# Performance work log

Measured on AMD Instinct MI355X. Metric: run time of the kernel, lower is better.

The kernel has to match this reference:

```python
import jax, jax.numpy as jnp
import numpy as np


def setup_inputs() -> dict:
    key = jax.random.key(0)
    ks = jax.random.split(key, 9)
    B = 1024
    s = 0.05
    return {
        "x": jax.random.normal(ks[0], (B, 1024), dtype=jnp.float32),
        "u1": jax.random.normal(ks[1], (8, 8, 16), dtype=jnp.float32) * s,
        "u2": jax.random.normal(ks[2], (8, 8, 16), dtype=jnp.float32) * s,
        "u3": jax.random.normal(ks[3], (16, 16, 16), dtype=jnp.float32) * s,
        "b2": jax.random.normal(ks[4], (16, 16, 16), dtype=jnp.float32) * s,
        "b1_core": jax.random.normal(ks[5], (16, 16), dtype=jnp.float32) * s,
        "bias1": jax.random.normal(ks[6], (8, 8, 16), dtype=jnp.float32) * s,
        "fc2_w": jax.random.normal(ks[7], (10, 1024), dtype=jnp.float32) * s,
        "fc2_b": jax.random.normal(ks[8], (10,), dtype=jnp.float32) * s,
    }


def reference(x, u1, u2, u3, b2, b1_core, bias1, fc2_w, fc2_b):
    batch = x.shape[0]
    t = x.reshape(batch, 8, 8, 16)                       # z a b c
    t = jnp.einsum('zabc,ade->zbcde', t, u1)             # (z,8,16,8,16)
    t = jnp.einsum('zabcd,def->zabcef', t, b2)           # (z,8,16,8,16,16)
    t = jnp.einsum('zabcde,afd->zbcef', t, u2)           # (z,16,8,16,8)
    t = jnp.einsum('zabcd,ce->zabde', t, b1_core)        # (z,16,8,8,16)
    t = jnp.einsum('zabcd,aed->zbce', t, u3)             # (z,8,8,16)
    t = t + bias1
    h = jax.nn.relu(t.reshape(batch, 1024))
    return h @ fc2_w.T + fc2_b
```

## Files before the change

kernel.cpp:

```cpp
#include <hip/hip_runtime.h>


using s16x8 = __attribute__((ext_vector_type(8))) short;
using f32x4 = __attribute__((ext_vector_type(4))) float;

__device__ inline short f2bf(float f) {
    unsigned u = __builtin_bit_cast(unsigned, f);
    u += 0x7fffu + ((u >> 16) & 1u);
    return (short)(u >> 16);
}

__global__ __launch_bounds__(256) void k_prep(
    const float* __restrict__ u1, const float* __restrict__ u2,
    const float* __restrict__ u3, const float* __restrict__ b2,
    const float* __restrict__ b1c, const float* __restrict__ fc2b,
    short* __restrict__ Wb, float* __restrict__ out) {
    const int blk = blockIdx.x;
    const int tid = threadIdx.x;

    __shared__ float b1s[256];
    __shared__ float u1s[128];
    __shared__ float u2s[64 * 17];
    __shared__ float u3s[4096];
    __shared__ float C2t[256 * 17];
    __shared__ float T1s[2048];
    __shared__ float T2s[64 * 17];
    const int d = blk >> 5;
    const int r = (blk >> 2) & 7;
    const int t0 = (blk & 3) * 4;

    if (tid < 40) {
        int idx = blk * 40 + tid;
        out[idx] = fc2b[idx % 10];
    }

    b1s[tid] = b1c[tid];
    {
        float4* dst = (float4*)u3s;
        const float4* src = (const float4*)u3;
#pragma unroll
        for (int q = 0; q < 4; ++q) dst[tid + 256 * q] = src[tid + 256 * q];
    }
    if (tid < 64) {
        const float4* src = (const float4*)&u2[tid * 16];
#pragma unroll
        for (int q = 0; q < 4; ++q) {
            float4 v = src[q];
            u2s[tid * 17 + q * 4 + 0] = v.x;
            u2s[tid * 17 + q * 4 + 1] = v.y;
            u2s[tid * 17 + q * 4 + 2] = v.z;
            u2s[tid * 17 + q * 4 + 3] = v.w;
        }
    }
    if (tid < 8) {
#pragma unroll
        for (int e = 0; e < 16; ++e)
            u1s[tid * 16 + e] = u1[(tid * 8 + d) * 16 + e];
    }
    float b2r[16];
    {
        const float4* src = (const float4*)&b2[tid * 16];
#pragma unroll
        for (int q = 0; q < 4; ++q) {
            float4 v = src[q];
            b2r[q * 4 + 0] = v.x; b2r[q * 4 + 1] = v.y;
            b2r[q * 4 + 2] = v.z; b2r[q * 4 + 3] = v.w;
        }
    }
    __syncthreads();

    {
        float accs[16] = {};
#pragma unroll
        for (int q = 0; q < 16; ++q) {
            const float bq = b2r[q];
#pragma unroll
            for (int s = 0; s < 16; ++s) accs[s] += bq * b1s[q * 16 + s];
        }
#pragma unroll
        for (int s = 0; s < 16; ++s) C2t[tid * 17 + s] = accs[s];
    }
    __syncthreads();

    {
        const int p = tid >> 4, s = tid & 15;
#pragma unroll
        for (int a = 0; a < 8; ++a) {
            float acc = 0.f;
#pragma unroll
            for (int e = 0; e < 16; ++e)
                acc += u1s[a * 16 + e] * C2t[(e * 16 + p) * 17 + s];
            T1s[a * 256 + tid] = acc;
        }
    }
    __syncthreads();

#pragma unroll
    for (int j = 0; j < 4; ++j) {
        int idx = tid + 256 * j;
        int ab = idx >> 4, s = idx & 15;
        int a = ab >> 3, b = ab & 7;
        float acc = 0.f;
#pragma unroll
        for (int p = 0; p < 16; ++p)
            acc += T1s[a * 256 + p * 16 + s] * u2s[(b * 8 + r) * 17 + p];
        T2s[ab * 17 + s] = acc;
    }
    __syncthreads();

    {
        const int j = tid >> 6;
        const int t = t0 + j;
        const int col0 = (tid & 63) * 16;
        const int ab = col0 >> 4;
        const float* t2p = &T2s[ab * 17];
        short* wrow = &Wb[(blk * 4 + j) * 1024 + col0];
        s16x8 v0, v1;
#pragma unroll
        for (int c = 0; c < 16; ++c) {
            const float* u3p = &u3s[c * 256 + t * 16];
            float acc = 0.f;
#pragma unroll
            for (int s = 0; s < 16; ++s) acc += t2p[s] * u3p[s];
            short bf = f2bf(acc);
            if (c < 8) v0[c] = bf; else v1[c - 8] = bf;
        }
        *(s16x8*)(wrow) = v0;
        *(s16x8*)(wrow + 8) = v1;
    }
}

#define LDK 264

__global__ __launch_bounds__(1024) void k_gemm(
    const float* __restrict__ X, const short* __restrict__ Wb,
    const float* __restrict__ bias, const float* __restrict__ W2,
    float* __restrict__ out) {
    extern __shared__ char dsm[];
    short (*As)[LDK] = (short(*)[LDK])dsm;
    short (*Bs)[LDK] = (short(*)[LDK])(dsm + 64 * LDK * 2);
    float* Hpf = (float*)dsm;
    __shared__ float W2s[10][64];

    const int tid = threadIdx.x;
    const int lane = tid & 63;
    const int w = tid >> 6;
    const int g = w >> 2;
    const int wr = (w >> 1) & 1, wc = w & 1;
    const int o0 = blockIdx.x * 64, z0 = blockIdx.y * 64;
    const int lr = lane & 15, lk = lane >> 4;

    if (tid < 160) {
        const int j = tid >> 4, c = (tid & 15) * 4;
        *(float4*)&W2s[j][c] = *(const float4*)&W2[j * 1024 + o0 + c];
    }

    const int srow = tid >> 4;
    const int scol = (tid & 15) * 16;
    const float* xp = &X[(z0 + srow) * 1024 + scol];
    const short* wp = &Wb[(o0 + srow) * 1024 + scol];

    f32x4 acc[2][2] = {};

    for (int it = 0; it < 4; ++it) {
        {
            const float* xi = xp + it * 256;
            const short* wi = wp + it * 256;
#pragma unroll
            for (int h = 0; h < 2; ++h) {
                float4 f0 = *(const float4*)(xi + h * 8);
                float4 f1 = *(const float4*)(xi + h * 8 + 4);
                s16x8 v;
                v[0] = f2bf(f0.x); v[1] = f2bf(f0.y);
                v[2] = f2bf(f0.z); v[3] = f2bf(f0.w);
                v[4] = f2bf(f1.x); v[5] = f2bf(f1.y);
                v[6] = f2bf(f1.z); v[7] = f2bf(f1.w);
                *(s16x8*)&As[srow][scol + h * 8] = v;
                *(s16x8*)&Bs[srow][scol + h * 8] = *(const s16x8*)(wi + h * 8);
            }
        }
        __syncthreads();
#pragma unroll
        for (int ks = 0; ks < 2; ++ks) {
            const int kb = g * 64 + ks * 32 + lk * 8;
            s16x8 a0 = *(const s16x8*)&As[wr * 32 + lr][kb];
            s16x8 a1 = *(const s16x8*)&As[wr * 32 + 16 + lr][kb];
            s16x8 b0 = *(const s16x8*)&Bs[wc * 32 + lr][kb];
            s16x8 b1 = *(const s16x8*)&Bs[wc * 32 + 16 + lr][kb];
            acc[0][0] = __builtin_amdgcn_mfma_f32_16x16x32_bf16(a0, b0, acc[0][0], 0, 0, 0);
            acc[0][1] = __builtin_amdgcn_mfma_f32_16x16x32_bf16(a0, b1, acc[0][1], 0, 0, 0);
            acc[1][0] = __builtin_amdgcn_mfma_f32_16x16x32_bf16(a1, b0, acc[1][0], 0, 0, 0);
            acc[1][1] = __builtin_amdgcn_mfma_f32_16x16x32_bf16(a1, b1, acc[1][1], 0, 0, 0);
        }
        __syncthreads();
    }

#pragma unroll
    for (int m = 0; m < 2; ++m)
#pragma unroll
        for (int n = 0; n < 2; ++n) {
            const int row = wr * 32 + m * 16 + lk * 4;
            const int col = wc * 32 + n * 16 + lr;
#pragma unroll
            for (int j = 0; j < 4; ++j)
                Hpf[(g * 64 + row + j) * 64 + col] = acc[m][n][j];
        }
    __syncthreads();

    const int hrow = tid >> 4;
    const int c4 = (tid & 15) * 4;
    float4 h0 = *(float4*)&Hpf[(0 * 64 + hrow) * 64 + c4];
    float4 h1 = *(float4*)&Hpf[(1 * 64 + hrow) * 64 + c4];
    float4 h2 = *(float4*)&Hpf[(2 * 64 + hrow) * 64 + c4];
    float4 h3 = *(float4*)&Hpf[(3 * 64 + hrow) * 64 + c4];
    float4 bv = *(const float4*)&bias[o0 + c4];
    float hv[4];
    hv[0] = fmaxf(h0.x + h1.x + h2.x + h3.x + bv.x, 0.f);
    hv[1] = fmaxf(h0.y + h1.y + h2.y + h3.y + bv.y, 0.f);
    hv[2] = fmaxf(h0.z + h1.z + h2.z + h3.z + bv.z, 0.f);
    hv[3] = fmaxf(h0.w + h1.w + h2.w + h3.w + bv.w, 0.f);

    float part[10];
#pragma unroll
    for (int jj = 0; jj < 10; ++jj) {
        part[jj] = hv[0] * W2s[jj][c4 + 0] + hv[1] * W2s[jj][c4 + 1]
                 + hv[2] * W2s[jj][c4 + 2] + hv[3] * W2s[jj][c4 + 3];
    }
#pragma unroll
    for (int jj = 0; jj < 10; ++jj) {
        float p = part[jj];
        p += __shfl_xor(p, 1);
        p += __shfl_xor(p, 2);
        p += __shfl_xor(p, 4);
        p += __shfl_xor(p, 8);
        if ((lane & 15) == 0) atomicAdd(&out[(z0 + hrow) * 10 + jj], p);
    }
}

extern "C" void kernel_launch(void* const* d_in, const int* in_sizes, int n_in,
                              void* d_out, int out_size, void* d_ws, size_t ws_size,
                              hipStream_t stream) {
    const float* x     = (const float*)d_in[0];
    const float* u1    = (const float*)d_in[1];
    const float* u2    = (const float*)d_in[2];
    const float* u3    = (const float*)d_in[3];
    const float* b2    = (const float*)d_in[4];
    const float* b1c   = (const float*)d_in[5];
    const float* bias1 = (const float*)d_in[6];
    const float* fc2w  = (const float*)d_in[7];
    const float* fc2b  = (const float*)d_in[8];
    float* out = (float*)d_out;

    short* Wb = (short*)d_ws;

    k_prep<<<256, 256, 0, stream>>>(u1, u2, u3, b2, b1c, fc2b, Wb, out);
    k_gemm<<<dim3(16, 16), 1024, 64 * LDK * 2 * 2, stream>>>(x, Wb, bias1,
                                                             fc2w, out);
}
```

Before: 32.16 us.

## Pre-convert x to swizzled bf16 and double-buffer GEMM with direct global-to-LDS loads

New measurement: 30.28 us. 5.9% less time.

```diff
diff --git a/kernel.cpp b/kernel.cpp
--- a/kernel.cpp
+++ b/kernel.cpp
@@ -10,13 +10,40 @@
     return (short)(u >> 16);
 }
 
+__device__ inline void gload16(const short* g, short* l) {
+    __builtin_amdgcn_global_load_lds(
+        (__attribute__((address_space(1))) void*)g,
+        (__attribute__((address_space(3))) void*)l, 16, 0, 0);
+}
+
 __global__ __launch_bounds__(256) void k_prep(
-    const float* __restrict__ u1, const float* __restrict__ u2,
-    const float* __restrict__ u3, const float* __restrict__ b2,
-    const float* __restrict__ b1c, const float* __restrict__ fc2b,
-    short* __restrict__ Wb, float* __restrict__ out) {
+    const float* __restrict__ x, const float* __restrict__ u1,
+    const float* __restrict__ u2, const float* __restrict__ u3,
+    const float* __restrict__ b2, const float* __restrict__ b1c,
+    const float* __restrict__ fc2b, short* __restrict__ Wb,
+    short* __restrict__ Xb, float* __restrict__ out) {
     const int blk = blockIdx.x;
     const int tid = threadIdx.x;
+
+    if (blk >= 256) {
+        const int base = (blk - 256) * 4096 + tid * 16;
+        const int z = base >> 10;
+        const int col = base & 1023;
+        const int c = col >> 3, g = c >> 4, c4 = c & 15, mz = z & 15;
+        short* xbase = &Xb[z * 1024 + g * 128];
+#pragma unroll
+        for (int h = 0; h < 2; ++h) {
+            float4 f0 = *(const float4*)&x[base + h * 8];
+            float4 f1 = *(const float4*)&x[base + h * 8 + 4];
+            s16x8 v;
+            v[0] = f2bf(f0.x); v[1] = f2bf(f0.y);
+            v[2] = f2bf(f0.z); v[3] = f2bf(f0.w);
+            v[4] = f2bf(f1.x); v[5] = f2bf(f1.y);
+            v[6] = f2bf(f1.z); v[7] = f2bf(f1.w);
+            *(s16x8*)(xbase + ((c4 + h) ^ mz) * 8) = v;
+        }
+        return;
+    }
 
     __shared__ float b1s[256];
     __shared__ float u1s[128];
@@ -110,11 +137,11 @@
 
     {
         const int j = tid >> 6;
+        const int o = blk * 4 + j;
         const int t = t0 + j;
         const int col0 = (tid & 63) * 16;
         const int ab = col0 >> 4;
         const float* t2p = &T2s[ab * 17];
-        short* wrow = &Wb[(blk * 4 + j) * 1024 + col0];
         s16x8 v0, v1;
 #pragma unroll
         for (int c = 0; c < 16; ++c) {
@@ -125,115 +152,103 @@
             short bf = f2bf(acc);
             if (c < 8) v0[c] = bf; else v1[c - 8] = bf;
         }
-        *(s16x8*)(wrow) = v0;
-        *(s16x8*)(wrow + 8) = v1;
-    }
-}
-
-#define LDK 264
-
-__global__ __launch_bounds__(1024) void k_gemm(
-    const float* __restrict__ X, const short* __restrict__ Wb,
+        const int cc = col0 >> 3;
+        const int g = cc >> 4, c4 = cc & 15, mo = o & 15;
+        short* wbase = &Wb[o * 1024 + g * 128];
+        *(s16x8*)(wbase + ((c4    ) ^ mo) * 8) = v0;
+        *(s16x8*)(wbase + ((c4 + 1) ^ mo) * 8) = v1;
+    }
+}
+
+__global__ __launch_bounds__(256) void k_gemm(
+    const short* __restrict__ Xb, const short* __restrict__ Wb,
     const float* __restrict__ bias, const float* __restrict__ W2,
     float* __restrict__ out) {
-    extern __shared__ char dsm[];
-    short (*As)[LDK] = (short(*)[LDK])dsm;
-    short (*Bs)[LDK] = (short(*)[LDK])(dsm + 64 * LDK * 2);
-    float* Hpf = (float*)dsm;
+    __shared__ short AB[2][2][64][128];
     __shared__ float W2s[10][64];
-
     const int tid = threadIdx.x;
-    const int lane = tid & 63;
-    const int w = tid >> 6;
-    const int g = w >> 2;
-    const int wr = (w >> 1) & 1, wc = w & 1;
+    const int ln = tid & 63;
+    const int wv = tid >> 6, wr = wv >> 1, wc = wv & 1;
     const int o0 = blockIdx.x * 64, z0 = blockIdx.y * 64;
-    const int lr = lane & 15, lk = lane >> 4;
+    const int lr = ln & 15, lk = ln >> 4;
 
     if (tid < 160) {
         const int j = tid >> 4, c = (tid & 15) * 4;
         *(float4*)&W2s[j][c] = *(const float4*)&W2[j * 1024 + o0 + c];
     }
 
-    const int srow = tid >> 4;
-    const int scol = (tid & 15) * 16;
-    const float* xp = &X[(z0 + srow) * 1024 + scol];
-    const short* wp = &Wb[(o0 + srow) * 1024 + scol];
+#define STAGE(buf, k0)                                                        \
+    do {                                                                      \
+        _Pragma("unroll")                                                     \
+        for (int q = 0; q < 4; ++q) {                                         \
+            const int rr = (wv * 4 + q) * 4 + lk;                             \
+            gload16(&Xb[(z0 + rr) * 1024 + (k0) + lr * 8],                    \
+                    &AB[buf][0][(wv * 4 + q) * 4][0]);                        \
+            gload16(&Wb[(o0 + rr) * 1024 + (k0) + lr * 8],                    \
+                    &AB[buf][1][(wv * 4 + q) * 4][0]);                        \
+        }                                                                     \
+    } while (0)
 
     f32x4 acc[2][2] = {};
-
-    for (int it = 0; it < 4; ++it) {
-        {
-            const float* xi = xp + it * 256;
-            const short* wi = wp + it * 256;
-#pragma unroll
-            for (int h = 0; h < 2; ++h) {
-                float4 f0 = *(const float4*)(xi + h * 8);
-                float4 f1 = *(const float4*)(xi + h * 8 + 4);
-                s16x8 v;
-                v[0] = f2bf(f0.x); v[1] = f2bf(f0.y);
-                v[2] = f2bf(f0.z); v[3] = f2bf(f0.w);
-                v[4] = f2bf(f1.x); v[5] = f2bf(f1.y);
-                v[6] = f2bf(f1.z); v[7] = f2bf(f1.w);
-                *(s16x8*)&As[srow][scol + h * 8] = v;
-                *(s16x8*)&Bs[srow][scol + h * 8] = *(const s16x8*)(wi + h * 8);
-            }
-        }
-        __syncthreads();
-#pragma unroll
-        for (int ks = 0; ks < 2; ++ks) {
-            const int kb = g * 64 + ks * 32 + lk * 8;
-            s16x8 a0 = *(const s16x8*)&As[wr * 32 + lr][kb];
-            s16x8 a1 = *(const s16x8*)&As[wr * 32 + 16 + lr][kb];
-            s16x8 b0 = *(const s16x8*)&Bs[wc * 32 + lr][kb];
-            s16x8 b1 = *(const s16x8*)&Bs[wc * 32 + 16 + lr][kb];
+    STAGE(0, 0);
+
+    for (int t = 0; t < 8; ++t) {
+        const int cur = t & 1;
+        if (t < 7) {
+            STAGE(cur ^ 1, (t + 1) * 128);
+            asm volatile("s_waitcnt vmcnt(8)" ::: "memory");
+        } else {
+            asm volatile("s_waitcnt vmcnt(0)" ::: "memory");
+        }
+        __builtin_amdgcn_s_barrier();
+#pragma unroll
+        for (int ks = 0; ks < 4; ++ks) {
+            const int pa = (((ks * 4) + lk) ^ lr) * 8;
+            s16x8 a0 = *(const s16x8*)&AB[cur][0][wr * 32 + lr][pa];
+            s16x8 a1 = *(const s16x8*)&AB[cur][0][wr * 32 + 16 + lr][pa];
+            s16x8 b0 = *(const s16x8*)&AB[cur][1][wc * 32 + lr][pa];
+            s16x8 b1 = *(const s16x8*)&AB[cur][1][wc * 32 + 16 + lr][pa];
             acc[0][0] = __builtin_amdgcn_mfma_f32_16x16x32_bf16(a0, b0, acc[0][0], 0, 0, 0);
             acc[0][1] = __builtin_amdgcn_mfma_f32_16x16x32_bf16(a0, b1, acc[0][1], 0, 0, 0);
             acc[1][0] = __builtin_amdgcn_mfma_f32_16x16x32_bf16(a1, b0, acc[1][0], 0, 0, 0);
             acc[1][1] = __builtin_amdgcn_mfma_f32_16x16x32_bf16(a1, b1, acc[1][1], 0, 0, 0);
         }
-        __syncthreads();
-    }
-
+        __builtin_amdgcn_s_barrier();
+        __builtin_amdgcn_sched_barrier(0);
+    }
+#undef STAGE
+
+    float* Ht = (float*)AB;
 #pragma unroll
     for (int m = 0; m < 2; ++m)
 #pragma unroll
         for (int n = 0; n < 2; ++n) {
             const int row = wr * 32 + m * 16 + lk * 4;
             const int col = wc * 32 + n * 16 + lr;
+            const float bv = bias[o0 + col];
 #pragma unroll
             for (int j = 0; j < 4; ++j)
-                Hpf[(g * 64 + row + j) * 64 + col] = acc[m][n][j];
-        }
-    __syncthreads();
-
-    const int hrow = tid >> 4;
-    const int c4 = (tid & 15) * 4;
-    float4 h0 = *(float4*)&Hpf[(0 * 64 + hrow) * 64 + c4];
-    float4 h1 = *(float4*)&Hpf[(1 * 64 + hrow) * 64 + c4];
-    float4 h2 = *(float4*)&Hpf[(2 * 64 + hrow) * 64 + c4];
-    float4 h3 = *(float4*)&Hpf[(3 * 64 + hrow) * 64 + c4];
-    float4 bv = *(const float4*)&bias[o0 + c4];
-    float hv[4];
-    hv[0] = fmaxf(h0.x + h1.x + h2.x + h3.x + bv.x, 0.f);
-    hv[1] = fmaxf(h0.y + h1.y + h2.y + h3.y + bv.y, 0.f);
-    hv[2] = fmaxf(h0.z + h1.z + h2.z + h3.z + bv.z, 0.f);
-    hv[3] = fmaxf(h0.w + h1.w + h2.w + h3.w + bv.w, 0.f);
-
+                Ht[(row + j) * 68 + col] = fmaxf(acc[m][n][j] + bv, 0.f);
+        }
+    __syncthreads();
+
+    const int zr = tid >> 2, q = tid & 3;
     float part[10];
 #pragma unroll
-    for (int jj = 0; jj < 10; ++jj) {
-        part[jj] = hv[0] * W2s[jj][c4 + 0] + hv[1] * W2s[jj][c4 + 1]
-                 + hv[2] * W2s[jj][c4 + 2] + hv[3] * W2s[jj][c4 + 3];
+    for (int jj = 0; jj < 10; ++jj) part[jj] = 0.f;
+#pragma unroll
+    for (int cc = 0; cc < 16; ++cc) {
+        const int cl = q + 4 * cc;
+        const float hv = Ht[zr * 68 + cl];
+#pragma unroll
+        for (int jj = 0; jj < 10; ++jj) part[jj] += hv * W2s[jj][cl];
     }
 #pragma unroll
     for (int jj = 0; jj < 10; ++jj) {
         float p = part[jj];
         p += __shfl_xor(p, 1);
         p += __shfl_xor(p, 2);
-        p += __shfl_xor(p, 4);
-        p += __shfl_xor(p, 8);
-        if ((lane & 15) == 0) atomicAdd(&out[(z0 + hrow) * 10 + jj], p);
+        if (q == 0) atomicAdd(&out[(z0 + zr) * 10 + jj], p);
     }
 }
 
@@ -252,8 +267,8 @@
     float* out = (float*)d_out;
 
     short* Wb = (short*)d_ws;
-
-    k_prep<<<256, 256, 0, stream>>>(u1, u2, u3, b2, b1c, fc2b, Wb, out);
-    k_gemm<<<dim3(16, 16), 1024, 64 * LDK * 2 * 2, stream>>>(x, Wb, bias1,
-                                                             fc2w, out);
-}
+    short* Xb = (short*)((char*)d_ws + 2u * 1024u * 1024u);
+
+    k_prep<<<512, 256, 0, stream>>>(x, u1, u2, u3, b2, b1c, fc2b, Wb, Xb, out);
+    k_gemm<<<dim3(16, 16), 256, 0, stream>>>(Xb, Wb, bias1, fc2w, out);
+}
```
